# Optimization experiments

Hardware: AMD Instinct MI355X
Metric: run time of the kernel (lower is better)

Reference implementation:

```python
import jax, jax.numpy as jnp
import numpy as np

B, S, D, H, F = 4, 1024, 2048, 16, 8192
HD = D // H  # head dim = 128
EPS = 1e-5


def layer_norm(x, w, b):
    mu = jnp.mean(x, axis=-1, keepdims=True)
    var = jnp.mean(jnp.square(x - mu), axis=-1, keepdims=True)
    return (x - mu) * jax.lax.rsqrt(var + EPS) * w + b


def setup_inputs() -> dict:
    key = jax.random.key(0)
    ks = jax.random.split(key, 12)
    s = 0.02  # realistic init scale for weights
    return {
        "x": jax.random.normal(ks[0], (B, S, D), jnp.float32),
        "attention_mask": jnp.zeros((B, 1, 1, S), jnp.float32),
        "wq": jax.random.normal(ks[1], (D, D), jnp.float32) * s,
        "bq": jax.random.normal(ks[2], (D,), jnp.float32) * s,
        "wk": jax.random.normal(ks[3], (D, D), jnp.float32) * s,
        "bk": jax.random.normal(ks[4], (D,), jnp.float32) * s,
        "wv": jax.random.normal(ks[5], (D, D), jnp.float32) * s,
        "bv": jax.random.normal(ks[6], (D,), jnp.float32) * s,
        "wo": jax.random.normal(ks[7], (D, D), jnp.float32) * s,
        "bo": jax.random.normal(ks[8], (D,), jnp.float32) * s,
        "ln1_w": jnp.ones((D,), jnp.float32),
        "ln1_b": jnp.zeros((D,), jnp.float32),
        "wi": jax.random.normal(ks[9], (F, D), jnp.float32) * s,
        "bi": jax.random.normal(ks[10], (F,), jnp.float32) * s,
        "wo2": jax.random.normal(ks[11], (D, F), jnp.float32) * s,
        "bo2": jnp.zeros((D,), jnp.float32),
        "ln2_w": jnp.ones((D,), jnp.float32),
        "ln2_b": jnp.zeros((D,), jnp.float32),
    }


def reference(x, attention_mask, wq, bq, wk, bk, wv, bv, wo, bo,
              ln1_w, ln1_b, wi, bi, wo2, bo2, ln2_w, ln2_b):
    # --- self attention ---
    q = (jnp.einsum('bsd,ed->bse', x, wq) + bq).reshape(B, S, H, HD).transpose(0, 2, 1, 3)
    k = (jnp.einsum('bsd,ed->bse', x, wk) + bk).reshape(B, S, H, HD).transpose(0, 2, 1, 3)
    v = (jnp.einsum('bsd,ed->bse', x, wv) + bv).reshape(B, S, H, HD).transpose(0, 2, 1, 3)
    scores = jnp.einsum('bhqd,bhkd->bhqk', q, k) / jnp.sqrt(jnp.float32(HD))
    scores = scores + attention_mask  # additive mask, broadcast over heads/query
    probs = jax.nn.softmax(scores, axis=-1)
    ctx = jnp.einsum('bhqk,bhkd->bhqd', probs, v)
    ctx = ctx.transpose(0, 2, 1, 3).reshape(B, S, D)
    # --- attention output: dense + bias + residual + LayerNorm ---
    attn_out = layer_norm(jnp.einsum('bsd,ed->bse', ctx, wo) + bo + x, ln1_w, ln1_b)
    # --- FFN: intermediate dense + bias, GELU, output dense + bias + residual + LN ---
    inter = jnp.einsum('bsd,fd->bsf', attn_out, wi) + bi
    h = jax.nn.gelu(inter, approximate=False)
    out = layer_norm(jnp.einsum('bsf,df->bsd', h, wo2) + bo2 + attn_out, ln2_w, ln2_b)
    return out
```

## Files before the change

### kernel.cpp

```cpp
#include <hip/hip_runtime.h>
#include <hip/hip_bf16.h>
#include <cstdint>
#include <cstddef>

typedef __attribute__((ext_vector_type(8))) short short8;
typedef __attribute__((ext_vector_type(4))) float f32x4;

#define DEV static __device__ __forceinline__

constexpr int kS = 1024, kD = 2048, kH = 16, kHD = 128, kF = 8192;
constexpr int kM = 4096;
constexpr float kEPS = 1e-5f;

constexpr size_t SZ_DD   = (size_t)kD * kD * 2;
constexpr size_t SZ_FD   = (size_t)kF * kD * 2;
constexpr size_t SZ_MD16 = (size_t)kM * kD * 2;
constexpr size_t SZ_MD32 = (size_t)kM * kD * 4;
constexpr size_t OFF_WQ  = 0;
constexpr size_t OFF_WK  = OFF_WQ + SZ_DD;
constexpr size_t OFF_WV  = OFF_WK + SZ_DD;
constexpr size_t OFF_WO  = OFF_WV + SZ_DD;
constexpr size_t OFF_WI  = OFF_WO + SZ_DD;
constexpr size_t OFF_WO2 = OFF_WI + SZ_FD;
constexpr size_t OFF_XB  = OFF_WO2 + SZ_FD;
constexpr size_t OFF_Q   = OFF_XB + SZ_MD16;
constexpr size_t OFF_K   = OFF_Q + SZ_MD16;
constexpr size_t OFF_V   = OFF_K + SZ_MD16;
constexpr size_t OFF_H   = OFF_XB;
constexpr size_t OFF_CTX = OFF_V + SZ_MD16;
constexpr size_t OFF_Y1  = OFF_CTX + SZ_MD16;
constexpr size_t OFF_A1B = OFF_Y1 + SZ_MD32;
constexpr size_t OFF_Y2  = OFF_A1B + SZ_MD16;
constexpr size_t WS_NEED = OFF_Y2 + SZ_MD32;

DEV void gload16(const void* g, void* l) {
  __builtin_amdgcn_global_load_lds(
      (const __attribute__((address_space(1))) unsigned int*)g,
      (__attribute__((address_space(3))) unsigned int*)l, 16, 0, 0);
}

__global__ void cvt_all(const float* __restrict__ x,  const float* __restrict__ wq,
                        const float* __restrict__ wk, const float* __restrict__ wv,
                        const float* __restrict__ wo, const float* __restrict__ wi,
                        const float* __restrict__ wo2,
                        const float* __restrict__ bq, const float* __restrict__ bk,
                        const float* __restrict__ bv,
                        __hip_bfloat16* __restrict__ outw, float* __restrict__ bqkv) {
  constexpr int M1 = 1 << 20;
  constexpr int NW = 14 * M1;
  int stride = gridDim.x * blockDim.x;
  for (int i = blockIdx.x * blockDim.x + threadIdx.x; i < NW + 1536; i += stride) {
    if (i < NW) {
      const float* src; int off;
      if (i < 4 * M1)       { src = (i < M1) ? wq : (i < 2 * M1) ? wk : (i < 3 * M1) ? wv : wo;
                              off = i & (M1 - 1); }
      else if (i < 8 * M1)  { src = wi;  off = i - 4 * M1; }
      else if (i < 12 * M1) { src = wo2; off = i - 8 * M1; }
      else                  { src = x;   off = i - 12 * M1; }
      float4 v = reinterpret_cast<const float4*>(src)[off];
      union { ushort4 u; __hip_bfloat16 h[4]; } o;
      o.h[0] = __float2bfloat16(v.x);
      o.h[1] = __float2bfloat16(v.y);
      o.h[2] = __float2bfloat16(v.z);
      o.h[3] = __float2bfloat16(v.w);
      reinterpret_cast<ushort4*>(outw)[i] = o.u;
    } else {
      int j = i - NW;
      const float* src = (j < 512) ? bq : (j < 1024) ? bk : bv;
      reinterpret_cast<float4*>(bqkv)[j] =
          reinterpret_cast<const float4*>(src)[j & 511];
    }
  }
}

template <int MODE>
__global__ __launch_bounds__(512, 2)
void gemm256(const __hip_bfloat16* __restrict__ A,
             const __hip_bfloat16* __restrict__ Bt,
             const float* __restrict__ bias,
             float* __restrict__ out0, float* __restrict__ out1,
             void* __restrict__ outb,
             int M, int N, int K, int kLen) {
  __shared__ __align__(16) char lds[131072];
  const int tid = threadIdx.x;
  const int lane = tid & 63, w = tid >> 6;
  const int wm = w >> 2, wn = w & 3;
  const int hw = w >> 2;
  const int lg = lane >> 4, lr = lane & 15;
  const int gy = M >> 8, gx = N >> 8;
  const int nwg = gridDim.x, orig = blockIdx.x;
  const int l = (orig & 7) * (nwg >> 3) + (orig >> 3);
  const int tilesPer = gx * gy;
  const int spl = l / tilesPer;
  const int rem = l - spl * tilesPer;
  const int bx = rem / gy, by = rem - bx * gy;
  const int m0 = by * 256, n0 = bx * 256;
  const int k0 = spl * kLen;
  const int NT = kLen >> 6;

  const char* gs[8];
  #pragma unroll
  for (int h = 0; h < 4; ++h) {
    const __hip_bfloat16* src = (h < 2) ? A : Bt;
    const int r0 = ((h < 2) ? m0 : n0) + (h & 1) * 128;
    #pragma unroll
    for (int i = 0; i < 2; ++i) {
      int c = i * 512 + tid;
      int row = c >> 3, slot = c & 7;
      gs[h * 2 + i] =
          (const char*)(src + (size_t)(r0 + row) * K + k0 + (slot ^ (row & 7)) * 8);
    }
  }

#define STAGE(P, H, TOFF)                                                          \
  {                                                                                \
    char* dstb = lds + (((H) < 2) ? 0 : 65536) + (P) * 32768 + ((H) & 1) * 16384;  \
    gload16(gs[(H) * 2 + 0] + (TOFF) * 128, dstb + (0 * 512 + tid) * 16);          \
    gload16(gs[(H) * 2 + 1] + (TOFF) * 128, dstb + (1 * 512 + tid) * 16);          \
  }

  auto ldA = [&](int P, int qm, int mr, int kk) {
    int row = qm * 128 + wm * 64 + mr * 16 + lr;
    return *reinterpret_cast<const short8*>(
        lds + P * 32768 + row * 128 + (((kk * 4 + lg) ^ (row & 7)) * 16));
  };
  auto ldB = [&](int P, int qn, int nr, int kk) {
    int row = qn * 128 + wn * 32 + nr * 16 + lr;
    return *reinterpret_cast<const short8*>(
        lds + 65536 + P * 32768 + row * 128 + (((kk * 4 + lg) ^ (row & 7)) * 16));
  };

  f32x4 acc[4][4][2] = {};

#define MFMA_HALF(p, kk, B)                                                     \
  _Pragma("unroll")                                                             \
  for (int mi = 0; mi < 4; ++mi)                                                \
    _Pragma("unroll")                                                           \
    for (int ni = 0; ni < 2; ++ni)                                              \
      acc[p][mi][ni] = __builtin_amdgcn_mfma_f32_16x16x32_bf16(                 \
          av[kk][mi], B[kk][ni], acc[p][mi][ni], 0, 0, 0);

#define WAIT_LGKM(n)                                                            \
  asm volatile("s_waitcnt lgkmcnt(" #n ")" ::: "memory");                       \
  __builtin_amdgcn_sched_barrier(0);

#define TILE_BODY(P, PF)                                                        \
  {                                                                             \
    asm volatile("s_waitcnt vmcnt(0)" ::: "memory");                            \
    __builtin_amdgcn_s_barrier();                                               \
    _Pragma("unroll")                                                           \
    for (int i = 0; i < 4; ++i) av[0][i] = ldA(P, hw, i, 0);                    \
    _Pragma("unroll")                                                           \
    for (int i = 0; i < 2; ++i) b0[0][i] = ldB(P, hw, i, 0);                    \
    _Pragma("unroll")                                                           \
    for (int i = 0; i < 4; ++i) av[1][i] = ldA(P, hw, i, 1);                    \
    _Pragma("unroll")                                                           \
    for (int i = 0; i < 2; ++i) b0[1][i] = ldB(P, hw, i, 1);                    \
    if (PF) { STAGE((P) ^ 1, 0, 1 + (P)) STAGE((P) ^ 1, 2, 1 + (P)) }           \
    WAIT_LGKM(6)                                                                \
    __builtin_amdgcn_s_setprio(1);                                              \
    MFMA_HALF(0, 0, b0)                                                         \
    WAIT_LGKM(0)                                                                \
    MFMA_HALF(0, 1, b0)                                                         \
    __builtin_amdgcn_s_setprio(0);                                              \
    _Pragma("unroll")                                                           \
    for (int i = 0; i < 2; ++i) b1[0][i] = ldB(P, 1 - hw, i, 0);                \
    _Pragma("unroll")                                                           \
    for (int i = 0; i < 2; ++i) b1[1][i] = ldB(P, 1 - hw, i, 1);                \
    if (PF) { STAGE((P) ^ 1, 3, 1 + (P)) STAGE((P) ^ 1, 1, 1 + (P)) }           \
    WAIT_LGKM(2)                                                                \
    __builtin_amdgcn_s_setprio(1);                                              \
    MFMA_HALF(1, 0, b1)                                                         \
    WAIT_LGKM(0)                                                                \
    MFMA_HALF(1, 1, b1)                                                         \
    __builtin_amdgcn_s_setprio(0);                                              \
    _Pragma("unroll")                                                           \
    for (int i = 0; i < 4; ++i) av[0][i] = ldA(P, 1 - hw, i, 0);                \
    _Pragma("unroll")                                                           \
    for (int i = 0; i < 4; ++i) av[1][i] = ldA(P, 1 - hw, i, 1);                \
    WAIT_LGKM(4)                                                                \
    __builtin_amdgcn_s_setprio(1);                                              \
    MFMA_HALF(2, 0, b1)                                                         \
    WAIT_LGKM(0)                                                                \
    MFMA_HALF(2, 1, b1)                                                         \
    __builtin_amdgcn_s_setprio(0);                                              \
    _Pragma("unroll")                                                           \
    for (int i = 0; i < 2; ++i) b0[0][i] = ldB(P, hw, i, 0);                    \
    _Pragma("unroll")                                                           \
    for (int i = 0; i < 2; ++i) b0[1][i] = ldB(P, hw, i, 1);                    \
    WAIT_LGKM(2)                                                                \
    __builtin_amdgcn_s_setprio(1);                                              \
    MFMA_HALF(3, 0, b0)                                                         \
    WAIT_LGKM(0)                                                                \
    MFMA_HALF(3, 1, b0)                                                         \
    __builtin_amdgcn_s_setprio(0);                                              \
  }

  STAGE(0, 0, 0) STAGE(0, 2, 0) STAGE(0, 3, 0) STAGE(0, 1, 0)

  for (int t2 = 0; t2 < NT; t2 += 2) {
    short8 av[2][4], b0[2][2], b1[2][2];
    TILE_BODY(0, true)
    TILE_BODY(1, (t2 + 2 < NT))
    #pragma unroll
    for (int j = 0; j < 8; ++j) gs[j] += 256;
  }
#undef TILE_BODY
#undef MFMA_HALF
#undef WAIT_LGKM
#undef STAGE

  #pragma unroll
  for (int p = 0; p < 4; ++p) {
    const int qm = (p < 2) ? hw : 1 - hw;
    const int qn = (p == 0 || p == 3) ? hw : 1 - hw;
    #pragma unroll
    for (int ni = 0; ni < 2; ++ni) {
      int col = n0 + qn * 128 + wn * 32 + ni * 16 + lr;
      float bvv = 0.f;
      if constexpr (MODE != 3) bvv = bias[col];
      #pragma unroll
      for (int mi = 0; mi < 4; ++mi) {
        int row0 = m0 + qm * 128 + wm * 64 + mi * 16 + lg * 4;
        #pragma unroll
        for (int r = 0; r < 4; ++r) {
          int row = row0 + r;
          float val = acc[p][mi][ni][r] + bvv;
          if constexpr (MODE == 0) {
            int which = col >> 11;
            int d = col & 2047;
            int hh = d >> 7, hd = d & 127;
            int bb = row >> 10, ss = row & 1023;
            __hip_bfloat16* base = (__hip_bfloat16*)outb + (size_t)which * ((size_t)kM * kD);
            base[(((size_t)(bb * kH + hh)) * kS + ss) * kHD + hd] = __float2bfloat16(val);
          } else if constexpr (MODE == 2) {
            float g = 0.5f * val * (1.0f + erff(val * 0.70710678118654752f));
            ((__hip_bfloat16*)outb)[(size_t)row * N + col] = __float2bfloat16(g);
          } else {
            float* o = spl ? out1 : out0;
            o[(size_t)row * N + col] = val;
          }
        }
      }
    }
  }
}

__global__ __launch_bounds__(512, 2)
void attn_fwd(const __hip_bfloat16* __restrict__ q,
              const __hip_bfloat16* __restrict__ k,
              const __hip_bfloat16* __restrict__ v,
              const float* __restrict__ mask,
              __hip_bfloat16* __restrict__ ctx) {
  __shared__ __align__(16) char Ks[2][64 * 256];
  __shared__ __align__(16) char Vt[2][128 * 128];
  __shared__ __align__(16) char Ps[8][2048];
  const int tid = threadIdx.x, lane = tid & 63, w = tid >> 6;
  const int lg = lane >> 4, lr = lane & 15;
  const int orig = blockIdx.x;
  const int l = (orig & 7) * 32 + (orig >> 3);
  const int qp = l & 3, bh = l >> 2;
  const int b = bh >> 4;
  const int s4 = tid >> 5, hd4 = tid & 31;

  short8 qf[2][4];
  #pragma unroll
  for (int s = 0; s < 2; ++s) {
    const __hip_bfloat16* qp_ =
        q + ((size_t)bh * kS + qp * 256 + s * 128 + w * 16 + lr) * kHD + lg * 8;
    #pragma unroll
    for (int kk = 0; kk < 4; ++kk)
      qf[s][kk] = *reinterpret_cast<const short8*>(qp_ + kk * 32);
  }

  auto stageK = [&](int bufi, int t) {
    #pragma unroll
    for (int i = 0; i < 2; ++i) {
      int c = i * 512 + tid;
      int row = c >> 4, slot = c & 15;
      gload16(k + ((size_t)bh * kS + t * 64 + row) * kHD + (slot ^ (row & 15)) * 8,
              Ks[bufi] + c * 16);
    }
  };
  union VU { uint2 u; ushort s[4]; };
  VU vr[4];
  auto loadV = [&](int t) {
    #pragma unroll
    for (int i = 0; i < 4; ++i)
      vr[i].u = *reinterpret_cast<const uint2*>(
          v + ((size_t)bh * kS + t * 64 + s4 * 4 + i) * kHD + hd4 * 4);
  };
  auto writeV = [&](int bufi) {
    #pragma unroll
    for (int j = 0; j < 4; ++j) {
      int hd = hd4 * 4 + j;
      ushort4 o4;
      o4.x = vr[0].s[j]; o4.y = vr[1].s[j]; o4.z = vr[2].s[j]; o4.w = vr[3].s[j];
      *reinterpret_cast<ushort4*>(
          Vt[bufi] + hd * 128 + (((s4 >> 1) ^ (hd & 7)) << 4) + ((s4 & 1) << 3)) = o4;
    }
  };

  f32x4 o[2][8] = {};
  float mrun[2][4], lrun[2][4];
  #pragma unroll
  for (int s = 0; s < 2; ++s)
    #pragma unroll
    for (int r = 0; r < 4; ++r) { mrun[s][r] = -1e30f; lrun[s][r] = 0.f; }
  const float scale = 0.08838834764831845f;

  stageK(0, 0);
  loadV(0);
  writeV(0);
  __syncthreads();

  int buf = 0;
  for (int t = 0; t < 16; ++t) {
    if (t + 1 < 16) { stageK(buf ^ 1, t + 1); loadV(t + 1); }

    float mv[4];
    #pragma unroll
    for (int j = 0; j < 4; ++j) mv[j] = mask[(size_t)b * kS + t * 64 + j * 16 + lr];

    #pragma unroll
    for (int s = 0; s < 2; ++s) {
      f32x4 sacc[4] = {};
      #pragma unroll
      for (int j = 0; j < 4; ++j) {
        int key = j * 16 + lr;
        #pragma unroll
        for (int kk = 0; kk < 4; ++kk) {
          short8 bfrag = *reinterpret_cast<const short8*>(
              Ks[buf] + key * 256 + (((kk * 4 + lg) ^ (key & 15)) * 16));
          sacc[j] = __builtin_amdgcn_mfma_f32_16x16x32_bf16(qf[s][kk], bfrag, sacc[j], 0, 0, 0);
        }
      }
      float sarr[4][4];
      #pragma unroll
      for (int j = 0; j < 4; ++j)
        #pragma unroll
        for (int r = 0; r < 4; ++r) sarr[j][r] = sacc[j][r] * scale + mv[j];
      #pragma unroll
      for (int r = 0; r < 4; ++r) {
        float tm = fmaxf(fmaxf(sarr[0][r], sarr[1][r]), fmaxf(sarr[2][r], sarr[3][r]));
        #pragma unroll
        for (int d = 1; d < 16; d <<= 1) tm = fmaxf(tm, __shfl_xor(tm, d));
        float mnew = fmaxf(mrun[s][r], tm);
        float alpha = __expf(mrun[s][r] - mnew);
        mrun[s][r] = mnew;
        float rs = 0.f;
        #pragma unroll
        for (int j = 0; j < 4; ++j) {
          float p = __expf(sarr[j][r] - mnew);
          sarr[j][r] = p;
          rs += p;
        }
        #pragma unroll
        for (int d = 1; d < 16; d <<= 1) rs += __shfl_xor(rs, d);
        lrun[s][r] = lrun[s][r] * alpha + rs;
        #pragma unroll
        for (int n = 0; n < 8; ++n) o[s][n][r] *= alpha;
      }
      #pragma unroll
      for (int r = 0; r < 4; ++r) {
        int qr = lg * 4 + r;
        #pragma unroll
        for (int j = 0; j < 4; ++j)
          *reinterpret_cast<__hip_bfloat16*>(
              Ps[w] + ((qr * 128 + (j * 16 + lr) * 2) ^ ((qr & 7) << 4))) =
              __float2bfloat16(sarr[j][r]);
      }
      #pragma unroll
      for (int kk2 = 0; kk2 < 2; ++kk2) {
        short8 pa = *reinterpret_cast<const short8*>(
            Ps[w] + ((lr * 128 + kk2 * 64 + lg * 16) ^ ((lr & 7) << 4)));
        #pragma unroll
        for (int n = 0; n < 8; ++n) {
          int hd = n * 16 + lr;
          short8 vb = *reinterpret_cast<const short8*>(
              Vt[buf] + hd * 128 + (((kk2 * 4 + lg) ^ (hd & 7)) * 16));
          o[s][n] = __builtin_amdgcn_mfma_f32_16x16x32_bf16(pa, vb, o[s][n], 0, 0, 0);
        }
      }
    }
    if (t + 1 < 16) writeV(buf ^ 1);
    __syncthreads();
    buf ^= 1;
  }

  const int h = bh & 15;
  #pragma unroll
  for (int s = 0; s < 2; ++s)
    #pragma unroll
    for (int r = 0; r < 4; ++r) {
      float inv = 1.0f / lrun[s][r];
      int srow = qp * 256 + s * 128 + w * 16 + lg * 4 + r;
      __hip_bfloat16* cp = ctx + ((size_t)b * kS + srow) * kD + h * 128 + lr;
      #pragma unroll
      for (int n = 0; n < 8; ++n) cp[n * 16] = __float2bfloat16(o[s][n][r] * inv);
    }
}

template <bool WB16>
__global__ void ln_fuse(const float* __restrict__ p0, const float* __restrict__ p1,
                        const float* __restrict__ bias, const float* __restrict__ res,
                        const float* __restrict__ w, const float* __restrict__ b,
                        float* __restrict__ outf, __hip_bfloat16* __restrict__ outb) {
  const int row = blockIdx.x, tid = threadIdx.x;
  const size_t base = (size_t)row * kD;
  float v[8];
  #pragma unroll
  for (int i = 0; i < 2; ++i) {
    int c4 = tid * 2 + i;
    float4 a  = reinterpret_cast<const float4*>(p0 + base)[c4];
    float4 bb = reinterpret_cast<const float4*>(p1 + base)[c4];
    float4 rr = reinterpret_cast<const float4*>(res + base)[c4];
    float4 bs = reinterpret_cast<const float4*>(bias)[c4];
    v[i * 4 + 0] = a.x + bb.x + rr.x + bs.x;
    v[i * 4 + 1] = a.y + bb.y + rr.y + bs.y;
    v[i * 4 + 2] = a.z + bb.z + rr.z + bs.z;
    v[i * 4 + 3] = a.w + bb.w + rr.w + bs.w;
  }
  float s = 0.f;
  #pragma unroll
  for (int i = 0; i < 8; ++i) s += v[i];
  #pragma unroll
  for (int off = 32; off > 0; off >>= 1) s += __shfl_down(s, off);
  __shared__ float r1[4], r2[4];
  if ((tid & 63) == 0) r1[tid >> 6] = s;
  __syncthreads();
  float mean = (r1[0] + r1[1] + r1[2] + r1[3]) * (1.0f / kD);
  float qv = 0.f;
  #pragma unroll
  for (int i = 0; i < 8; ++i) { float d = v[i] - mean; qv += d * d; }
  #pragma unroll
  for (int off = 32; off > 0; off >>= 1) qv += __shfl_down(qv, off);
  if ((tid & 63) == 0) r2[tid >> 6] = qv;
  __syncthreads();
  float rstd = rsqrtf((r2[0] + r2[1] + r2[2] + r2[3]) * (1.0f / kD) + kEPS);
  #pragma unroll
  for (int i = 0; i < 8; ++i) {
    int col = tid * 8 + i;
    float ov = (v[i] - mean) * rstd * w[col] + b[col];
    outf[base + col] = ov;
    if constexpr (WB16) outb[base + col] = __float2bfloat16(ov);
  }
}

extern "C" void kernel_launch(void* const* d_in, const int* in_sizes, int n_in,
                              void* d_out, int out_size, void* d_ws, size_t ws_size,
                              hipStream_t stream) {
  (void)in_sizes; (void)n_in; (void)out_size;
  if (ws_size < WS_NEED) return;
  const float* x    = (const float*)d_in[0];
  const float* mask = (const float*)d_in[1];
  const float* wq   = (const float*)d_in[2];
  const float* bq   = (const float*)d_in[3];
  const float* wk   = (const float*)d_in[4];
  const float* bk   = (const float*)d_in[5];
  const float* wv   = (const float*)d_in[6];
  const float* bv   = (const float*)d_in[7];
  const float* wo   = (const float*)d_in[8];
  const float* bo   = (const float*)d_in[9];
  const float* l1w  = (const float*)d_in[10];
  const float* l1b  = (const float*)d_in[11];
  const float* wi   = (const float*)d_in[12];
  const float* bi   = (const float*)d_in[13];
  const float* wo2  = (const float*)d_in[14];
  const float* bo2  = (const float*)d_in[15];
  const float* l2w  = (const float*)d_in[16];
  const float* l2b  = (const float*)d_in[17];

  char* ws = (char*)d_ws;
  __hip_bfloat16* wqb  = (__hip_bfloat16*)(ws + OFF_WQ);
  __hip_bfloat16* wob  = (__hip_bfloat16*)(ws + OFF_WO);
  __hip_bfloat16* wib  = (__hip_bfloat16*)(ws + OFF_WI);
  __hip_bfloat16* wo2b = (__hip_bfloat16*)(ws + OFF_WO2);
  __hip_bfloat16* xb   = (__hip_bfloat16*)(ws + OFF_XB);
  __hip_bfloat16* qb   = (__hip_bfloat16*)(ws + OFF_Q);
  __hip_bfloat16* kb2  = (__hip_bfloat16*)(ws + OFF_K);
  __hip_bfloat16* vb2  = (__hip_bfloat16*)(ws + OFF_V);
  __hip_bfloat16* hb   = (__hip_bfloat16*)(ws + OFF_H);
  __hip_bfloat16* ctxb = (__hip_bfloat16*)(ws + OFF_CTX);
  __hip_bfloat16* a1b  = (__hip_bfloat16*)(ws + OFF_A1B);
  float* y1   = (float*)(ws + OFF_Y1);
  float* y2   = (float*)(ws + OFF_Y2);
  float* f2p  = (float*)(ws + OFF_WQ);
  float* bqkv = (float*)(ws + OFF_Y2);

  cvt_all<<<2048, 256, 0, stream>>>(x, wq, wk, wv, wo, wi, wo2, bq, bk, bv, wqb, bqkv);

  dim3 blk(512);
  gemm256<0><<<dim3(384), blk, 0, stream>>>(
      xb, wqb, bqkv, nullptr, nullptr, qb, kM, 6144, kD, kD);
  attn_fwd<<<dim3(256), dim3(512), 0, stream>>>(qb, kb2, vb2, mask, ctxb);
  gemm256<3><<<dim3(256), blk, 0, stream>>>(
      ctxb, wob, nullptr, y1, y2, nullptr, kM, kD, kD, kD / 2);
  ln_fuse<true><<<kM, 256, 0, stream>>>(y1, y2, bo, x, l1w, l1b, y1, a1b);
  gemm256<2><<<dim3(512), blk, 0, stream>>>(
      a1b, wib, bi, nullptr, nullptr, hb, kM, kF, kD, kD);
  gemm256<3><<<dim3(256), blk, 0, stream>>>(
      hb, wo2b, nullptr, y2, f2p, nullptr, kM, kD, kF, kF / 2);
  ln_fuse<false><<<kM, 256, 0, stream>>>(y2, f2p, bo2, y1, l2w, l2b, (float*)d_out, nullptr);
}
```

Before: 604.6 us.

## Overlap wi/wo2 weight conversion with attention kernel compute

Moves the fp32-to-bf16 conversion of the two large FFN weight matrices out of the standalone conversion kernel and into the attention kernel's main loop. Each attention block loads and stores a slice of the weights per key tile. The goal is to hide this memory-bound conversion behind the compute-bound attention MFMA work instead of paying for it serially. The cost is higher register pressure and extra memory traffic inside attention, which could hurt its occupancy or stall its loads.

```diff
diff --git a/kernel.cpp b/kernel.cpp
--- a/kernel.cpp
+++ b/kernel.cpp
@@ -41,29 +41,26 @@
 
 __global__ void cvt_all(const float* __restrict__ x,  const float* __restrict__ wq,
                         const float* __restrict__ wk, const float* __restrict__ wv,
-                        const float* __restrict__ wo, const float* __restrict__ wi,
-                        const float* __restrict__ wo2,
+                        const float* __restrict__ wo,
                         const float* __restrict__ bq, const float* __restrict__ bk,
                         const float* __restrict__ bv,
                         __hip_bfloat16* __restrict__ outw, float* __restrict__ bqkv) {
   constexpr int M1 = 1 << 20;
-  constexpr int NW = 14 * M1;
+  constexpr int NW = 6 * M1;
   int stride = gridDim.x * blockDim.x;
   for (int i = blockIdx.x * blockDim.x + threadIdx.x; i < NW + 1536; i += stride) {
     if (i < NW) {
-      const float* src; int off;
-      if (i < 4 * M1)       { src = (i < M1) ? wq : (i < 2 * M1) ? wk : (i < 3 * M1) ? wv : wo;
-                              off = i & (M1 - 1); }
-      else if (i < 8 * M1)  { src = wi;  off = i - 4 * M1; }
-      else if (i < 12 * M1) { src = wo2; off = i - 8 * M1; }
-      else                  { src = x;   off = i - 12 * M1; }
+      const float* src; int off; int dst;
+      if (i < 4 * M1) { src = (i < M1) ? wq : (i < 2 * M1) ? wk : (i < 3 * M1) ? wv : wo;
+                        off = i & (M1 - 1); dst = i; }
+      else            { src = x; off = i - 4 * M1; dst = i + 8 * M1; }
       float4 v = reinterpret_cast<const float4*>(src)[off];
       union { ushort4 u; __hip_bfloat16 h[4]; } o;
       o.h[0] = __float2bfloat16(v.x);
       o.h[1] = __float2bfloat16(v.y);
       o.h[2] = __float2bfloat16(v.z);
       o.h[3] = __float2bfloat16(v.w);
-      reinterpret_cast<ushort4*>(outw)[i] = o.u;
+      reinterpret_cast<ushort4*>(outw)[dst] = o.u;
     } else {
       int j = i - NW;
       const float* src = (j < 512) ? bq : (j < 1024) ? bk : bv;
@@ -251,7 +248,9 @@
               const __hip_bfloat16* __restrict__ k,
               const __hip_bfloat16* __restrict__ v,
               const float* __restrict__ mask,
-              __hip_bfloat16* __restrict__ ctx) {
+              __hip_bfloat16* __restrict__ ctx,
+              const float* __restrict__ wi, const float* __restrict__ wo2,
+              __hip_bfloat16* __restrict__ outw ) {
   __shared__ __align__(16) char Ks[2][64 * 256];
   __shared__ __align__(16) char Vt[2][128 * 128];
   __shared__ __align__(16) char Ps[8][2048];
@@ -300,6 +299,29 @@
           Vt[bufi] + hd * 128 + (((s4 >> 1) ^ (hd & 7)) << 4) + ((s4 & 1) << 3)) = o4;
     }
   };
+  float4 cw[4];
+  auto cvLoad = [&](int t) {
+    int g0 = ((orig * 16 + t) * 512 + tid) * 4;
+    #pragma unroll
+    for (int j = 0; j < 4; ++j) {
+      int g = g0 + j;
+      const float* src = (g < (4 << 20)) ? wi : wo2;
+      int off = g & ((4 << 20) - 1);
+      cw[j] = reinterpret_cast<const float4*>(src)[off];
+    }
+  };
+  auto cvStore = [&](int t) {
+    int g0 = ((orig * 16 + t) * 512 + tid) * 4;
+    #pragma unroll
+    for (int j = 0; j < 4; ++j) {
+      union { ushort4 u; __hip_bfloat16 h[4]; } o4;
+      o4.h[0] = __float2bfloat16(cw[j].x);
+      o4.h[1] = __float2bfloat16(cw[j].y);
+      o4.h[2] = __float2bfloat16(cw[j].z);
+      o4.h[3] = __float2bfloat16(cw[j].w);
+      reinterpret_cast<ushort4*>(outw)[(4 << 20) + g0 + j] = o4.u;
+    }
+  };
 
   f32x4 o[2][8] = {};
   float mrun[2][4], lrun[2][4];
@@ -317,6 +339,7 @@
   int buf = 0;
   for (int t = 0; t < 16; ++t) {
     if (t + 1 < 16) { stageK(buf ^ 1, t + 1); loadV(t + 1); }
+    cvLoad(t);
 
     float mv[4];
     #pragma unroll
@@ -383,6 +406,7 @@
         }
       }
     }
+    cvStore(t);
     if (t + 1 < 16) writeV(buf ^ 1);
     __syncthreads();
     buf ^= 1;
@@ -488,12 +512,12 @@
   float* f2p  = (float*)(ws + OFF_WQ);
   float* bqkv = (float*)(ws + OFF_Y2);
 
-  cvt_all<<<2048, 256, 0, stream>>>(x, wq, wk, wv, wo, wi, wo2, bq, bk, bv, wqb, bqkv);
+  cvt_all<<<2048, 256, 0, stream>>>(x, wq, wk, wv, wo, bq, bk, bv, wqb, bqkv);
 
   dim3 blk(512);
   gemm256<0><<<dim3(384), blk, 0, stream>>>(
       xb, wqb, bqkv, nullptr, nullptr, qb, kM, 6144, kD, kD);
-  attn_fwd<<<dim3(256), dim3(512), 0, stream>>>(qb, kb2, vb2, mask, ctxb);
+  attn_fwd<<<dim3(256), dim3(512), 0, stream>>>(qb, kb2, vb2, mask, ctxb, wi, wo2, wqb);
   gemm256<3><<<dim3(256), blk, 0, stream>>>(
       ctxb, wob, nullptr, y1, y2, nullptr, kM, kD, kD, kD / 2);
   ln_fuse<true><<<kM, 256, 0, stream>>>(y1, y2, bo, x, l1w, l1b, y1, a1b);
```

After: 594.6 us. Within noise of the previous version (-1.6%).
